# Performance work log

Measured on AMD Instinct MI355X. Metric: run time of the kernel, lower is better.

The kernel has to match this reference:

```python
import jax, jax.numpy as jnp
import numpy as np

N0, N1, N2 = 200000, 50000, 10000
D_IN, D_PROMPT, D_HID, D_OUT = 128, 64, 256, 2
E0, E1 = 800000, 160000


def _glorot(key, shape):
    fan_in, fan_out = shape[0], shape[1]
    lim = np.sqrt(6.0 / (fan_in + fan_out))
    return jax.random.uniform(key, shape, jnp.float32, -lim, lim)


def setup_inputs() -> dict:
    key = jax.random.key(0)
    ks = jax.random.split(key, 20)
    inp = {
        "features": jax.random.normal(ks[0], (N0, D_IN), jnp.float32),
        "membership_mask": jax.random.randint(ks[1], (N0,), 0, 2) > 0,
        "src0": jax.random.randint(ks[2], (E0,), 0, N0),
        "dst0": jax.random.randint(ks[3], (E0,), 0, N1),
        "src1": jax.random.randint(ks[4], (E1,), 0, N1),
        "dst1": jax.random.randint(ks[5], (E1,), 0, N2),
        "output_nodes_indices": jax.random.randint(ks[6], (N2,), 0, N2),
        # prompt MLPs
        "w_pin": _glorot(ks[7], (D_IN, D_PROMPT)),
        "b_pin": jnp.zeros((D_PROMPT,), jnp.float32),
        "w_pout": _glorot(ks[8], (D_IN, D_PROMPT)),
        "b_pout": jnp.zeros((D_PROMPT,), jnp.float32),
        # SAGEConv layer 0: (D_IN+D_PROMPT) -> D_HID
        "w_self0": _glorot(ks[9], (D_IN + D_PROMPT, D_HID)),
        "w_neigh0": _glorot(ks[10], (D_IN + D_PROMPT, D_HID)),
        "b0": jnp.zeros((D_HID,), jnp.float32),
        # SAGEConv layer 1: D_HID -> D_HID
        "w_self1": _glorot(ks[11], (D_HID, D_HID)),
        "w_neigh1": _glorot(ks[12], (D_HID, D_HID)),
        "b1": jnp.zeros((D_HID,), jnp.float32),
        # classifier
        "w_cls": _glorot(ks[13], (D_HID, D_OUT)),
        "b_cls": jnp.zeros((D_OUT,), jnp.float32),
    }
    return inp


def _sage_mean(h, src, dst, n_dst, w_self, w_neigh, b):
    # mean-aggregate src features into dst buckets (zero-degree -> 0, DGL semantics)
    agg = jax.ops.segment_sum(h[src], dst, num_segments=n_dst)
    deg = jax.ops.segment_sum(jnp.ones((src.shape[0],), h.dtype), dst, num_segments=n_dst)
    agg = agg / jnp.maximum(deg, 1.0)[:, None]
    return h[:n_dst] @ w_self + agg @ w_neigh + b


def reference(features, membership_mask, src0, dst0, src1, dst1, output_nodes_indices,
              w_pin, b_pin, w_pout, b_pout,
              w_self0, w_neigh0, b0, w_self1, w_neigh1, b1, w_cls, b_cls):
    p_in = jax.nn.relu(features @ w_pin + b_pin)
    p_out = jax.nn.relu(features @ w_pout + b_pout)
    sel = jnp.where(membership_mask[:, None], p_in, p_out)
    h = jnp.concatenate([features, sel], axis=1)          # [N0, D_IN+D_PROMPT]
    h = jax.nn.relu(_sage_mean(h, src0, dst0, N1, w_self0, w_neigh0, b0))  # [N1, D_HID]
    h = _sage_mean(h, src1, dst1, N2, w_self1, w_neigh1, b1)               # [N2, D_HID]
    logits = h @ w_cls + b_cls                             # [N2, D_OUT]
    return logits
```

## Files before the change

kernel.cpp:

```cpp
#include <hip/hip_runtime.h>


#define N0v 200000
#define N1v 50000
#define N2v 10000
#define E0v 800000
#define E1v 160000
#define TB0 49
#define TB1 10
#define TBL (TB0 + TB1)
#define NTILE 3125
#define PGRID 512

using u16 = unsigned short;
typedef __attribute__((ext_vector_type(8))) short short8;
typedef __attribute__((ext_vector_type(4))) float f32x4;

__device__ __forceinline__ float b2f(u16 u) {
    union { unsigned int i; float f; } v; v.i = ((unsigned int)u) << 16; return v.f;
}
__device__ __forceinline__ u16 f2b(float f) {
    union { float f; unsigned int i; } v; v.f = f;
    return (u16)((v.i + 0x7fffu + ((v.i >> 16) & 1u)) >> 16);
}
__device__ __forceinline__ void split2(float f, u16& h, u16& l) {
    h = f2b(f);
    l = f2b(f - b2f(h));
}

__global__ void k_prep(const unsigned* mask, int* flag,
                       const float* w_pin, const float* w_pout, u16* WTph, u16* WTpl,
                       const float* ws0, const float* wn0, u16* WT0h, u16* WT0l,
                       const float* ws1, const float* wn1, u16* WT1h, u16* WT1l,
                       const float* bc, float* outp,
                       const int* __restrict__ dst0, const int* __restrict__ dst1,
                       int* cnt0, int* cnt1, int* rk0, int* rk1) {
    const int R0 = 50000;
    const int R1 = R0 + 128 * 128;
    const int R2 = R1 + 256 * 384;
    const int R3 = R2 + 256 * 512;
    const int R4 = R3 + 2 * N2v;
    const int R5 = R4 + E0v;
    const int R6 = R5 + E1v;
    for (int i = blockIdx.x * blockDim.x + threadIdx.x; i < R6;
         i += gridDim.x * blockDim.x) {
        if (i < R0) {
            if (mask[i] > 1u) atomicOr(flag, 1);
        } else if (i < R1) {
            int j = i - R0, n = j >> 7, k = j & 127;
            float f = (n < 64) ? w_pin[k * 64 + n] : w_pout[k * 64 + (n - 64)];
            split2(f, WTph[j], WTpl[j]);
        } else if (i < R2) {
            int j = i - R1, n = j / 384, k = j % 384;
            float f = (k < 192) ? ws0[k * 256 + n] : wn0[(k - 192) * 256 + n];
            split2(f, WT0h[j], WT0l[j]);
        } else if (i < R3) {
            int j = i - R2, n = j >> 9, k = j & 511;
            float f = (k < 256) ? ws1[k * 256 + n] : wn1[(k - 256) * 256 + n];
            split2(f, WT1h[j], WT1l[j]);
        } else if (i < R4) {
            int j = i - R3;
            outp[j] = bc[j & 1];
        } else if (i < R5) {
            int e = i - R4;
            rk0[e] = atomicAdd(&cnt0[dst0[e]], 1);
        } else {
            int e = i - R5;
            rk1[e] = atomicAdd(&cnt1[dst1[e]], 1);
        }
    }
}

__global__ __launch_bounds__(256) void k_scan_a(const int* __restrict__ cnt0,
                                                int* __restrict__ off0,
                                                const int* __restrict__ cnt1,
                                                int* __restrict__ off1,
                                                int* __restrict__ tsum) {
    __shared__ int sd[256];
    const int t = threadIdx.x;
    const int blk = blockIdx.x;
    const int g1 = (blk >= TB0);
    const int b = g1 ? blk - TB0 : blk;
    const int n = g1 ? N2v : N1v;
    const int* cnt = g1 ? cnt1 : cnt0;
    int* off = g1 ? off1 : off0;
    const int i0 = b * 1024 + t * 4;
    int c[4] = {0, 0, 0, 0};
    if (i0 + 3 < n) {
        *(int4*)c = *(const int4*)&cnt[i0];
    } else {
        for (int j = 0; j < 4; j++) if (i0 + j < n) c[j] = cnt[i0 + j];
    }
    int s = c[0] + c[1] + c[2] + c[3];
    sd[t] = s;
    __syncthreads();
#pragma unroll
    for (int d = 1; d < 256; d <<= 1) {
        int v = (t >= d) ? sd[t - d] : 0;
        __syncthreads();
        sd[t] += v;
        __syncthreads();
    }
    int run = sd[t] - s;
    int o4[4];
#pragma unroll
    for (int j = 0; j < 4; j++) { o4[j] = run; run += c[j]; }
    if (i0 + 3 < n) *(int4*)&off[i0] = *(const int4*)o4;
    else for (int j = 0; j < 4; j++) if (i0 + j < n) off[i0 + j] = o4[j];
    if (t == 255) tsum[blk] = sd[255];
}

__global__ __launch_bounds__(256) void k_scan_c(int* __restrict__ off0,
                                                int* __restrict__ off1,
                                                const int* __restrict__ tsum) {
    __shared__ int lbase;
    const int t = threadIdx.x;
    const int blk = blockIdx.x;
    const int g1 = (blk >= TB0);
    const int b = g1 ? blk - TB0 : blk;
    const int n = g1 ? N2v : N1v;
    int* off = g1 ? off1 : off0;
    if (t < 64) {
        int v = (t < TBL) ? tsum[t] : 0;
        int incl = v;
#pragma unroll
        for (int d = 1; d < 64; d <<= 1) {
            int u = __shfl_up(incl, d);
            if (t >= d) incl += u;
        }
        int total0 = __shfl(incl, TB0 - 1);
        if (t == blk) lbase = (incl - v) - (g1 ? total0 : 0);
    }
    __syncthreads();
    const int base = lbase;
    const int i0 = b * 1024 + t * 4;
    if (i0 + 3 < n) {
        int4 v = *(int4*)&off[i0];
        v.x += base; v.y += base; v.z += base; v.w += base;
        *(int4*)&off[i0] = v;
    } else {
        for (int j = 0; j < 4; j++) if (i0 + j < n) off[i0 + j] += base;
    }
    if (blk == 0 && t == 0) { off0[N1v] = E0v; off1[N2v] = E1v; }
}

__global__ __launch_bounds__(256) void k_scatter2(
    const int* __restrict__ src0, const int* __restrict__ dst0,
    const int* __restrict__ off0, const int* __restrict__ rk0, int* __restrict__ ei0,
    const int* __restrict__ src1, const int* __restrict__ dst1,
    const int* __restrict__ off1, const int* __restrict__ rk1, int* __restrict__ ei1) {
    const int part = blockIdx.x & 7;
    const int chunk = blockIdx.x >> 3;
    const int nch = gridDim.x >> 3;
    {
        const int per = (E0v + nch - 1) / nch;
        const int i1 = min((chunk + 1) * per, E0v);
        for (int i = chunk * per + (int)threadIdx.x; i < i1; i += 256) {
            int d = dst0[i];
            if (d / 6250 == part) ei0[off0[d] + rk0[i]] = src0[i];
        }
    }
    {
        const int per = (E1v + nch - 1) / nch;
        const int i1 = min((chunk + 1) * per, E1v);
        for (int i = chunk * per + (int)threadIdx.x; i < i1; i += 256) {
            int d = dst1[i];
            if (d / 1250 == part) ei1[off1[d] + rk1[i]] = src1[i];
        }
    }
}

__global__ __launch_bounds__(256, 2) void k_gemm_p(
    const float* __restrict__ A, const u16* __restrict__ Bh, const u16* __restrict__ Bl,
    const float* __restrict__ b_pin, const float* __restrict__ b_pout,
    const void* maskp, const int* __restrict__ flag, u16* __restrict__ G) {
    __shared__ __align__(16) u16 STG[2][8448];
    __shared__ __align__(16) u16 EPI[8704];
    const int t = threadIdx.x;
    const int lane = t & 63, w = t >> 6;
    const int m = lane & 15, q = lane >> 4;
    const int colbase = w * 32;
    const int r15 = t >> 4, ch = t & 15;
    const int k0s = ch >> 2, q2s = ch & 3;

    const size_t ba = (size_t)(colbase + m) * 128 + q * 8;
    const size_t bb = (size_t)(colbase + 16 + m) * 128 + q * 8;
    short8 BfA[4][2], BfB[4][2];
#pragma unroll
    for (int k0 = 0; k0 < 4; k0++) {
        BfA[k0][0] = *(const short8*)&Bh[ba + k0 * 32];
        BfA[k0][1] = *(const short8*)&Bl[ba + k0 * 32];
        BfB[k0][0] = *(const short8*)&Bh[bb + k0 * 32];
        BfB[k0][1] = *(const short8*)&Bl[bb + k0 * 32];
    }
    const int fl = *flag;
    float bv0, bv1;
    {
        int c0 = colbase + m, c1 = colbase + 16 + m;
        bv0 = (c0 < 64) ? b_pin[c0] : b_pout[c0 - 64];
        bv1 = (c1 < 64) ? b_pin[c1] : b_pout[c1 - 64];
    }

    float4 va[8];
    {
        const float* ap = &A[(size_t)(blockIdx.x * 64 + r15) * 128 + ch * 8];
#pragma unroll
        for (int p = 0; p < 4; p++) {
            va[2 * p]     = *(const float4*)(ap + (size_t)p * 16 * 128);
            va[2 * p + 1] = *(const float4*)(ap + (size_t)p * 16 * 128 + 4);
        }
    }

    int buf = 0;
    for (int bm = blockIdx.x; bm < NTILE; bm += PGRID, buf ^= 1) {
        const int r0 = bm * 64;
        u16* stg = STG[buf];
#pragma unroll
        for (int p = 0; p < 4; p++) {
            u16 h8[8];
            h8[0] = f2b(va[2 * p].x); h8[1] = f2b(va[2 * p].y);
            h8[2] = f2b(va[2 * p].z); h8[3] = f2b(va[2 * p].w);
            h8[4] = f2b(va[2 * p + 1].x); h8[5] = f2b(va[2 * p + 1].y);
            h8[6] = f2b(va[2 * p + 1].z); h8[7] = f2b(va[2 * p + 1].w);
            *(uint4*)&stg[((p * 4 + k0s) * 66 + 16 * q2s + r15) * 8] = *(const uint4*)h8;
        }
        __syncthreads();

        if (bm + PGRID < NTILE) {
            const float* ap = &A[(size_t)((bm + PGRID) * 64 + r15) * 128 + ch * 8];
#pragma unroll
            for (int p = 0; p < 4; p++) {
                va[2 * p]     = *(const float4*)(ap + (size_t)p * 16 * 128);
                va[2 * p + 1] = *(const float4*)(ap + (size_t)p * 16 * 128 + 4);
            }
        }
        bool mk0, mk1;
        {
            const int ra = r0 + (t >> 3), rb = ra + 32;
            if (fl) {
                mk0 = ((const unsigned char*)maskp)[ra] != 0;
                mk1 = ((const unsigned char*)maskp)[rb] != 0;
            } else {
                mk0 = ((const int*)maskp)[ra] != 0;
                mk1 = ((const int*)maskp)[rb] != 0;
            }
        }

        f32x4 acc[4][2] = {};
#pragma unroll
        for (int k0 = 0; k0 < 4; k0++) {
#pragma unroll
            for (int mi = 0; mi < 4; mi++) {
                short8 af = *(const short8*)&stg[((mi * 4 + k0) * 66 + lane) * 8];
                acc[mi][0] = __builtin_amdgcn_mfma_f32_16x16x32_bf16(af, BfA[k0][0], acc[mi][0], 0, 0, 0);
                acc[mi][0] = __builtin_amdgcn_mfma_f32_16x16x32_bf16(af, BfA[k0][1], acc[mi][0], 0, 0, 0);
                acc[mi][1] = __builtin_amdgcn_mfma_f32_16x16x32_bf16(af, BfB[k0][0], acc[mi][1], 0, 0, 0);
                acc[mi][1] = __builtin_amdgcn_mfma_f32_16x16x32_bf16(af, BfB[k0][1], acc[mi][1], 0, 0, 0);
            }
        }

#pragma unroll
        for (int mi = 0; mi < 4; mi++)
#pragma unroll
            for (int r = 0; r < 4; r++) {
                float v0 = acc[mi][0][r] + bv0;
                float v1 = acc[mi][1][r] + bv1;
                v0 = v0 > 0.f ? v0 : 0.f;
                v1 = v1 > 0.f ? v1 : 0.f;
                EPI[(mi * 16 + q * 4 + r) * 136 + colbase + m] = f2b(v0);
                EPI[(mi * 16 + q * 4 + r) * 136 + colbase + 16 + m] = f2b(v1);
            }
        __syncthreads();

        {
            const int c8 = t & 7;
            const int rt = t >> 3;
            *(uint4*)&G[(size_t)(r0 + rt) * 192 + 128 + c8 * 8] =
                *(const uint4*)&EPI[rt * 136 + (mk0 ? 0 : 64) + c8 * 8];
            *(uint4*)&G[(size_t)(r0 + 32 + rt) * 192 + 128 + c8 * 8] =
                *(const uint4*)&EPI[(32 + rt) * 136 + (mk1 ? 0 : 64) + c8 * 8];
        }
#pragma unroll
        for (int p = 0; p < 4; p++) {
            uint4 v = *(const uint4*)&stg[((p * 4 + k0s) * 66 + 16 * q2s + r15) * 8];
            *(uint4*)&G[(size_t)(r0 + r15 + 16 * p) * 192 + ch * 8] = v;
        }
    }
}

template <int MODE, int KT, int SEGA0, int MT>
__global__ __launch_bounds__(256, 3) void k_g(
    const u16* __restrict__ A0, int s0, const u16* __restrict__ A1, int s1,
    const u16* __restrict__ Bh, const u16* __restrict__ Bl,
    const float* __restrict__ bias,
    u16* __restrict__ CH, float* __restrict__ outp, const float* __restrict__ wc,
    int M) {
    constexpr int MI = MT / 16;
    __shared__ __align__(16) u16 LA[MI * KT * 66 * 8];
    const int t = threadIdx.x;
    const int bm = blockIdx.x >> 1, bn = blockIdx.x & 1;
    const int lane = t & 63, w = t >> 6;
    const int m = lane & 15, q = lane >> 4;
    const int r0 = bm * MT;
    const int colbase = bn * 128 + w * 32;
    const int K = KT * 32;

    {
        constexpr int TPR = 256 / MT;
        constexpr int SPT = KT / TPR;
        const int rr = t / TPR, sub = t & (TPR - 1);
        int arow = r0 + rr; if (arow >= M) arow = M - 1;
        const int mi = rr >> 4, r15 = rr & 15;
#pragma unroll
        for (int s = 0; s < SPT; s++) {
            const int kc = sub * SPT + s;
#pragma unroll
            for (int q2 = 0; q2 < 4; q2++) {
                const int c = kc * 32 + q2 * 8;
                uint4 v = (c < SEGA0)
                              ? *(const uint4*)&A0[(size_t)arow * s0 + c]
                              : *(const uint4*)&A1[(size_t)arow * s1 + (c - SEGA0)];
                *(uint4*)&LA[((mi * KT + kc) * 66 + 16 * q2 + r15) * 8] = v;
            }
        }
    }
    __syncthreads();

    const size_t ba = (size_t)(colbase + m) * K + q * 8;
    const size_t bb = (size_t)(colbase + 16 + m) * K + q * 8;

    f32x4 acc[MI][2] = {};
#pragma unroll 1
    for (int kb = 0; kb < KT; kb += 4) {
#pragma unroll
        for (int k0 = 0; k0 < 4; k0++) {
            const size_t ko = (size_t)(kb + k0) * 32;
            short8 b0h = *(const short8*)&Bh[ba + ko];
            short8 b0l = *(const short8*)&Bl[ba + ko];
            short8 b1h = *(const short8*)&Bh[bb + ko];
            short8 b1l = *(const short8*)&Bl[bb + ko];
#pragma unroll
            for (int mi = 0; mi < MI; mi++) {
                short8 af = *(const short8*)&LA[((mi * KT + kb + k0) * 66 + lane) * 8];
                acc[mi][0] = __builtin_amdgcn_mfma_f32_16x16x32_bf16(af, b0h, acc[mi][0], 0, 0, 0);
                acc[mi][0] = __builtin_amdgcn_mfma_f32_16x16x32_bf16(af, b0l, acc[mi][0], 0, 0, 0);
                acc[mi][1] = __builtin_amdgcn_mfma_f32_16x16x32_bf16(af, b1h, acc[mi][1], 0, 0, 0);
                acc[mi][1] = __builtin_amdgcn_mfma_f32_16x16x32_bf16(af, b1l, acc[mi][1], 0, 0, 0);
            }
        }
    }

    if (MODE == 1) {
        float bv[2];
#pragma unroll
        for (int nt = 0; nt < 2; nt++) bv[nt] = bias[colbase + nt * 16 + m];
        __syncthreads();
#pragma unroll
        for (int mi = 0; mi < MI; mi++)
#pragma unroll
            for (int nt = 0; nt < 2; nt++)
#pragma unroll
                for (int r = 0; r < 4; r++) {
                    float v = acc[mi][nt][r] + bv[nt];
                    v = v > 0.f ? v : 0.f;
                    LA[(mi * 16 + q * 4 + r) * 136 + w * 32 + nt * 16 + m] = f2b(v);
                }
        __syncthreads();
        const int c16 = t & 15;
#pragma unroll
        for (int pass = 0; pass < MT / 16; pass++) {
            const int rt = pass * 16 + (t >> 4);
            const int row = r0 + rt;
            if (row < M) {
                *(uint4*)&CH[(size_t)row * 256 + bn * 128 + c16 * 8] =
                    *(const uint4*)&LA[rt * 136 + c16 * 8];
            }
        }
    } else {
        const int ca = colbase + m, cb = colbase + 16 + m;
        const float bva = bias[ca], bvb = bias[cb];
        const float w0a = wc[ca * 2], w1a = wc[ca * 2 + 1];
        const float w0b = wc[cb * 2], w1b = wc[cb * 2 + 1];
#pragma unroll
        for (int mi = 0; mi < MI; mi++) {
#pragma unroll
            for (int r = 0; r < 4; r++) {
                int row = r0 + mi * 16 + q * 4 + r;
                float va = acc[mi][0][r] + bva;
                float vb = acc[mi][1][r] + bvb;
                float p0 = va * w0a + vb * w0b;
                float p1 = va * w1a + vb * w1b;
#pragma unroll
                for (int s = 1; s < 16; s <<= 1) {
                    p0 += __shfl_xor(p0, s);
                    p1 += __shfl_xor(p1, s);
                }
                if (m == 0 && row < M) {
                    atomicAdd(&outp[row * 2], p0);
                    atomicAdd(&outp[row * 2 + 1], p1);
                }
            }
        }
    }
}

__global__ void k_agg0(const u16* __restrict__ G, const int* __restrict__ off,
                       const int* __restrict__ eidx, u16* __restrict__ aggH) {
    int wid = (blockIdx.x * blockDim.x + threadIdx.x) >> 6;
    int lane = threadIdx.x & 63;
    if (wid >= N1v) return;
    int b = off[wid], e = off[wid + 1];
    float f0 = 0.f, f1 = 0.f, p0 = 0.f;
    for (int base = b; base < e; base += 64) {
        int li = base + lane;
        int idx = eidx[li < e ? li : (e - 1)];
        int nch = e - base; if (nch > 64) nch = 64;
        int j = 0;
        for (; j + 4 <= nch; j += 4) {
            int sa = __shfl(idx, j), sb = __shfl(idx, j + 1);
            int sc = __shfl(idx, j + 2), sd = __shfl(idx, j + 3);
            const u16* ra = &G[(size_t)sa * 192];
            const u16* rb = &G[(size_t)sb * 192];
            const u16* rc = &G[(size_t)sc * 192];
            const u16* rd = &G[(size_t)sd * 192];
            unsigned fa = *(const unsigned*)&ra[2 * lane];
            unsigned fb = *(const unsigned*)&rb[2 * lane];
            unsigned fc = *(const unsigned*)&rc[2 * lane];
            unsigned fd = *(const unsigned*)&rd[2 * lane];
            u16 pa = ra[128 + lane], pb = rb[128 + lane];
            u16 pc = rc[128 + lane], pd = rd[128 + lane];
            f0 += b2f((u16)fa) + b2f((u16)fb) + b2f((u16)fc) + b2f((u16)fd);
            f1 += b2f((u16)(fa >> 16)) + b2f((u16)(fb >> 16)) +
                  b2f((u16)(fc >> 16)) + b2f((u16)(fd >> 16));
            p0 += b2f(pa) + b2f(pb) + b2f(pc) + b2f(pd);
        }
        for (; j < nch; j++) {
            int s = __shfl(idx, j);
            const u16* row = &G[(size_t)s * 192];
            unsigned fv = *(const unsigned*)&row[2 * lane];
            f0 += b2f((u16)fv);
            f1 += b2f((u16)(fv >> 16));
            p0 += b2f(row[128 + lane]);
        }
    }
    int deg = e - b;
    float inv = 1.0f / (float)(deg > 1 ? deg : 1);
    size_t rb2 = (size_t)wid * 192;
    *(unsigned*)&aggH[rb2 + 2 * lane] =
        (unsigned)f2b(f0 * inv) | ((unsigned)f2b(f1 * inv) << 16);
    aggH[rb2 + 128 + lane] = f2b(p0 * inv);
}

__global__ void k_agg1(const u16* __restrict__ h1H, const int* __restrict__ off,
                       const int* __restrict__ eidx, u16* __restrict__ aggH) {
    int wid = (blockIdx.x * blockDim.x + threadIdx.x) >> 6;
    int lane = threadIdx.x & 63;
    if (wid >= N2v) return;
    int b = off[wid], e = off[wid + 1];
    float a0 = 0.f, a1 = 0.f, a2 = 0.f, a3 = 0.f;
    for (int base = b; base < e; base += 64) {
        int li = base + lane;
        int idx = eidx[li < e ? li : (e - 1)];
        int nch = e - base; if (nch > 64) nch = 64;
        int j = 0;
        for (; j + 4 <= nch; j += 4) {
            int sa = __shfl(idx, j), sb = __shfl(idx, j + 1);
            int sc = __shfl(idx, j + 2), sd = __shfl(idx, j + 3);
            const u16* ra = &h1H[(size_t)sa * 256];
            const u16* rb = &h1H[(size_t)sb * 256];
            const u16* rc = &h1H[(size_t)sc * 256];
            const u16* rd = &h1H[(size_t)sd * 256];
            unsigned va0 = *(const unsigned*)&ra[2 * lane];
            unsigned vb0 = *(const unsigned*)&rb[2 * lane];
            unsigned vc0 = *(const unsigned*)&rc[2 * lane];
            unsigned vd0 = *(const unsigned*)&rd[2 * lane];
            unsigned va1 = *(const unsigned*)&ra[128 + 2 * lane];
            unsigned vb1 = *(const unsigned*)&rb[128 + 2 * lane];
            unsigned vc1 = *(const unsigned*)&rc[128 + 2 * lane];
            unsigned vd1 = *(const unsigned*)&rd[128 + 2 * lane];
            a0 += b2f((u16)va0) + b2f((u16)vb0) + b2f((u16)vc0) + b2f((u16)vd0);
            a1 += b2f((u16)(va0 >> 16)) + b2f((u16)(vb0 >> 16)) +
                  b2f((u16)(vc0 >> 16)) + b2f((u16)(vd0 >> 16));
            a2 += b2f((u16)va1) + b2f((u16)vb1) + b2f((u16)vc1) + b2f((u16)vd1);
            a3 += b2f((u16)(va1 >> 16)) + b2f((u16)(vb1 >> 16)) +
                  b2f((u16)(vc1 >> 16)) + b2f((u16)(vd1 >> 16));
        }
        for (; j < nch; j++) {
            int s = __shfl(idx, j);
            const u16* row = &h1H[(size_t)s * 256];
            unsigned v0 = *(const unsigned*)&row[2 * lane];
            unsigned v1 = *(const unsigned*)&row[128 + 2 * lane];
            a0 += b2f((u16)v0); a1 += b2f((u16)(v0 >> 16));
            a2 += b2f((u16)v1); a3 += b2f((u16)(v1 >> 16));
        }
    }
    int deg = e - b;
    float inv = 1.0f / (float)(deg > 1 ? deg : 1);
    size_t rb2 = (size_t)wid * 256;
    *(unsigned*)&aggH[rb2 + 2 * lane] =
        (unsigned)f2b(a0 * inv) | ((unsigned)f2b(a1 * inv) << 16);
    *(unsigned*)&aggH[rb2 + 128 + 2 * lane] =
        (unsigned)f2b(a2 * inv) | ((unsigned)f2b(a3 * inv) << 16);
}

extern "C" void kernel_launch(void* const* d_in, const int* in_sizes, int n_in,
                              void* d_out, int out_size, void* d_ws, size_t ws_size,
                              hipStream_t stream) {
    const float* features = (const float*)d_in[0];
    const void* maskp     = d_in[1];
    const int* src0       = (const int*)d_in[2];
    const int* dst0       = (const int*)d_in[3];
    const int* src1       = (const int*)d_in[4];
    const int* dst1       = (const int*)d_in[5];
    const float* w_pin    = (const float*)d_in[7];
    const float* b_pin    = (const float*)d_in[8];
    const float* w_pout   = (const float*)d_in[9];
    const float* b_pout   = (const float*)d_in[10];
    const float* w_self0  = (const float*)d_in[11];
    const float* w_neigh0 = (const float*)d_in[12];
    const float* b0       = (const float*)d_in[13];
    const float* w_self1  = (const float*)d_in[14];
    const float* w_neigh1 = (const float*)d_in[15];
    const float* b1       = (const float*)d_in[16];
    const float* w_cls    = (const float*)d_in[17];
    const float* b_cls    = (const float*)d_in[18];
    float* out = (float*)d_out;
    (void)in_sizes; (void)n_in; (void)out_size; (void)ws_size;

    char* ws = (char*)d_ws;
    size_t o = 0;
    auto alloc = [&](size_t bytes) { size_t r = o; o += (bytes + 255) & ~(size_t)255; return r; };
    size_t o_flag = alloc(4);
    size_t o_cnt0 = alloc(N1v * 4);
    size_t o_cnt1 = alloc(N2v * 4);
    size_t zero_end = o;
    size_t o_G    = alloc((size_t)N0v * 192 * 2);
    size_t o_aggH = alloc((size_t)N1v * 192 * 2);
    size_t o_h1H  = alloc((size_t)N1v * 256 * 2);
    size_t o_ag1H = alloc((size_t)N2v * 256 * 2);
    size_t o_wtph = alloc(128 * 128 * 2), o_wtpl = alloc(128 * 128 * 2);
    size_t o_wt0h = alloc(256 * 384 * 2), o_wt0l = alloc(256 * 384 * 2);
    size_t o_wt1h = alloc(256 * 512 * 2), o_wt1l = alloc(256 * 512 * 2);
    size_t o_off0 = alloc((N1v + 1) * 4);
    size_t o_off1 = alloc((N2v + 1) * 4);
    size_t o_ei0  = alloc((size_t)E0v * 4);
    size_t o_ei1  = alloc((size_t)E1v * 4);
    size_t o_rk0  = alloc((size_t)E0v * 4);
    size_t o_rk1  = alloc((size_t)E1v * 4);
    size_t o_tsum = alloc(TBL * 4);

    int* flag = (int*)(ws + o_flag);
    int* cnt0 = (int*)(ws + o_cnt0);
    int* cnt1 = (int*)(ws + o_cnt1);
    u16* G     = (u16*)(ws + o_G);
    u16* aggH  = (u16*)(ws + o_aggH);
    u16* h1H   = (u16*)(ws + o_h1H);
    u16* ag1H  = (u16*)(ws + o_ag1H);
    u16* WTph = (u16*)(ws + o_wtph);
    u16* WTpl = (u16*)(ws + o_wtpl);
    u16* WT0h = (u16*)(ws + o_wt0h);
    u16* WT0l = (u16*)(ws + o_wt0l);
    u16* WT1h = (u16*)(ws + o_wt1h);
    u16* WT1l = (u16*)(ws + o_wt1l);
    int* off0 = (int*)(ws + o_off0);
    int* off1 = (int*)(ws + o_off1);
    int* ei0  = (int*)(ws + o_ei0);
    int* ei1  = (int*)(ws + o_ei1);
    int* rk0  = (int*)(ws + o_rk0);
    int* rk1  = (int*)(ws + o_rk1);
    int* tsum = (int*)(ws + o_tsum);

    hipMemsetAsync(ws + o_flag, 0, zero_end - o_flag, stream);

    k_prep<<<1024, 256, 0, stream>>>((const unsigned*)maskp, flag,
                                     w_pin, w_pout, WTph, WTpl,
                                     w_self0, w_neigh0, WT0h, WT0l,
                                     w_self1, w_neigh1, WT1h, WT1l,
                                     b_cls, out, dst0, dst1, cnt0, cnt1, rk0, rk1);

    k_scan_a<<<TBL, 256, 0, stream>>>(cnt0, off0, cnt1, off1, tsum);
    k_scan_c<<<TBL, 256, 0, stream>>>(off0, off1, tsum);

    k_scatter2<<<2048, 256, 0, stream>>>(src0, dst0, off0, rk0, ei0,
                                         src1, dst1, off1, rk1, ei1);

    k_gemm_p<<<PGRID, 256, 0, stream>>>(features, WTph, WTpl,
                                        b_pin, b_pout, maskp, flag, G);

    k_agg0<<<(N1v + 3) / 4, 256, 0, stream>>>(G, off0, ei0, aggH);

    k_g<1, 12, 192, 64><<<((N1v + 63) / 64) * 2, 256, 0, stream>>>(
        G, 192, aggH, 192, WT0h, WT0l, b0, h1H, nullptr, nullptr, N1v);

    k_agg1<<<(N2v + 3) / 4, 256, 0, stream>>>(h1H, off1, ei1, ag1H);

    k_g<3, 16, 256, 32><<<((N2v + 31) / 32) * 2, 256, 0, stream>>>(
        h1H, 256, ag1H, 256, WT1h, WT1l, b1, nullptr, out, w_cls, N2v);
}
```

Baseline: 413.2 us.

## Merge prompt GEMM with prep work into one heterogeneous kernel

Splits the old prep kernel so that mask-type detection runs in its own small kernel. Weight splitting, output init and edge counting move into extra blocks of the prompt GEMM kernel, so they run alongside the features GEMM instead of before it. The prompt weights are now split into hi/lo bf16 parts directly in registers inside the GEMM blocks, which removes the transposed prompt-weight buffers. The trade-off is one extra small launch plus strided global weight loads repeated by each GEMM block, and prep blocks compete with GEMM blocks for CUs.

```diff
diff --git a/kernel.cpp b/kernel.cpp
--- a/kernel.cpp
+++ b/kernel.cpp
@@ -11,6 +11,7 @@
 #define TBL (TB0 + TB1)
 #define NTILE 3125
 #define PGRID 512
+#define PREPB 768
 
 using u16 = unsigned short;
 typedef __attribute__((ext_vector_type(8))) short short8;
@@ -28,45 +29,178 @@
     l = f2b(f - b2f(h));
 }
 
-__global__ void k_prep(const unsigned* mask, int* flag,
-                       const float* w_pin, const float* w_pout, u16* WTph, u16* WTpl,
-                       const float* ws0, const float* wn0, u16* WT0h, u16* WT0l,
-                       const float* ws1, const float* wn1, u16* WT1h, u16* WT1l,
-                       const float* bc, float* outp,
-                       const int* __restrict__ dst0, const int* __restrict__ dst1,
-                       int* cnt0, int* cnt1, int* rk0, int* rk1) {
-    const int R0 = 50000;
-    const int R1 = R0 + 128 * 128;
-    const int R2 = R1 + 256 * 384;
-    const int R3 = R2 + 256 * 512;
-    const int R4 = R3 + 2 * N2v;
-    const int R5 = R4 + E0v;
-    const int R6 = R5 + E1v;
-    for (int i = blockIdx.x * blockDim.x + threadIdx.x; i < R6;
+__global__ void k_detect(const unsigned* mask, int* flag) {
+    for (int i = blockIdx.x * blockDim.x + threadIdx.x; i < 50000;
          i += gridDim.x * blockDim.x) {
-        if (i < R0) {
-            if (mask[i] > 1u) atomicOr(flag, 1);
-        } else if (i < R1) {
-            int j = i - R0, n = j >> 7, k = j & 127;
-            float f = (n < 64) ? w_pin[k * 64 + n] : w_pout[k * 64 + (n - 64)];
-            split2(f, WTph[j], WTpl[j]);
-        } else if (i < R2) {
-            int j = i - R1, n = j / 384, k = j % 384;
-            float f = (k < 192) ? ws0[k * 256 + n] : wn0[(k - 192) * 256 + n];
-            split2(f, WT0h[j], WT0l[j]);
-        } else if (i < R3) {
-            int j = i - R2, n = j >> 9, k = j & 511;
-            float f = (k < 256) ? ws1[k * 256 + n] : wn1[(k - 256) * 256 + n];
-            split2(f, WT1h[j], WT1l[j]);
-        } else if (i < R4) {
-            int j = i - R3;
-            outp[j] = bc[j & 1];
-        } else if (i < R5) {
-            int e = i - R4;
-            rk0[e] = atomicAdd(&cnt0[dst0[e]], 1);
-        } else {
-            int e = i - R5;
-            rk1[e] = atomicAdd(&cnt1[dst1[e]], 1);
+        if (mask[i] > 1u) atomicOr(flag, 1);
+    }
+}
+
+__global__ __launch_bounds__(256, 2) void k_mega(
+    const float* __restrict__ A, const float* __restrict__ w_pin,
+    const float* __restrict__ w_pout,
+    const float* __restrict__ b_pin, const float* __restrict__ b_pout,
+    const void* maskp, const int* __restrict__ flag, u16* __restrict__ G,
+    const float* __restrict__ ws0, const float* __restrict__ wn0,
+    u16* WT0h, u16* WT0l,
+    const float* __restrict__ ws1, const float* __restrict__ wn1,
+    u16* WT1h, u16* WT1l,
+    const float* __restrict__ bc, float* outp,
+    const int* __restrict__ dst0, const int* __restrict__ dst1,
+    int* cnt0, int* cnt1, int* rk0, int* rk1) {
+    __shared__ __align__(16) u16 STG[2][8448];
+    __shared__ __align__(16) u16 EPI[8704];
+    const int t = threadIdx.x;
+
+    if (blockIdx.x >= PGRID) {
+        const int R1 = 256 * 384;
+        const int R2 = R1 + 256 * 512;
+        const int R3 = R2 + 2 * N2v;
+        const int R4 = R3 + E0v;
+        const int R5 = R4 + E1v;
+        const int stride = PREPB * 256;
+        for (int i = (blockIdx.x - PGRID) * 256 + t; i < R5; i += stride) {
+            if (i < R1) {
+                int n = i / 384, k = i % 384;
+                float f = (k < 192) ? ws0[k * 256 + n] : wn0[(k - 192) * 256 + n];
+                split2(f, WT0h[i], WT0l[i]);
+            } else if (i < R2) {
+                int j = i - R1, n = j >> 9, k = j & 511;
+                float f = (k < 256) ? ws1[k * 256 + n] : wn1[(k - 256) * 256 + n];
+                split2(f, WT1h[j], WT1l[j]);
+            } else if (i < R3) {
+                int j = i - R2;
+                outp[j] = bc[j & 1];
+            } else if (i < R4) {
+                int e = i - R3;
+                rk0[e] = atomicAdd(&cnt0[dst0[e]], 1);
+            } else {
+                int e = i - R4;
+                rk1[e] = atomicAdd(&cnt1[dst1[e]], 1);
+            }
+        }
+        return;
+    }
+
+    const int lane = t & 63, w = t >> 6;
+    const int m = lane & 15, q = lane >> 4;
+    const int colbase = w * 32;
+    const int r15 = t >> 4, ch = t & 15;
+    const int k0s = ch >> 2, q2s = ch & 3;
+
+    short8 BfA[4][2], BfB[4][2];
+    {
+        const int c0 = colbase + m, c1 = colbase + 16 + m;
+        const float* wp0 = (c0 < 64) ? w_pin : w_pout;
+        const int cc0 = (c0 < 64) ? c0 : c0 - 64;
+        const float* wp1 = (c1 < 64) ? w_pin : w_pout;
+        const int cc1 = (c1 < 64) ? c1 : c1 - 64;
+#pragma unroll
+        for (int k0 = 0; k0 < 4; k0++) {
+            u16 h8[8], l8[8];
+#pragma unroll
+            for (int j = 0; j < 8; j++)
+                split2(wp0[(k0 * 32 + q * 8 + j) * 64 + cc0], h8[j], l8[j]);
+            BfA[k0][0] = *(const short8*)h8;
+            BfA[k0][1] = *(const short8*)l8;
+#pragma unroll
+            for (int j = 0; j < 8; j++)
+                split2(wp1[(k0 * 32 + q * 8 + j) * 64 + cc1], h8[j], l8[j]);
+            BfB[k0][0] = *(const short8*)h8;
+            BfB[k0][1] = *(const short8*)l8;
+        }
+    }
+    const int fl = *flag;
+    float bv0, bv1;
+    {
+        int c0 = colbase + m, c1 = colbase + 16 + m;
+        bv0 = (c0 < 64) ? b_pin[c0] : b_pout[c0 - 64];
+        bv1 = (c1 < 64) ? b_pin[c1] : b_pout[c1 - 64];
+    }
+
+    float4 va[8];
+    {
+        const float* ap = &A[(size_t)(blockIdx.x * 64 + r15) * 128 + ch * 8];
+#pragma unroll
+        for (int p = 0; p < 4; p++) {
+            va[2 * p]     = *(const float4*)(ap + (size_t)p * 16 * 128);
+            va[2 * p + 1] = *(const float4*)(ap + (size_t)p * 16 * 128 + 4);
+        }
+    }
+
+    int buf = 0;
+    for (int bm = blockIdx.x; bm < NTILE; bm += PGRID, buf ^= 1) {
+        const int r0 = bm * 64;
+        u16* stg = STG[buf];
+#pragma unroll
+        for (int p = 0; p < 4; p++) {
+            u16 h8[8];
+            h8[0] = f2b(va[2 * p].x); h8[1] = f2b(va[2 * p].y);
+            h8[2] = f2b(va[2 * p].z); h8[3] = f2b(va[2 * p].w);
+            h8[4] = f2b(va[2 * p + 1].x); h8[5] = f2b(va[2 * p + 1].y);
+            h8[6] = f2b(va[2 * p + 1].z); h8[7] = f2b(va[2 * p + 1].w);
+            *(uint4*)&stg[((p * 4 + k0s) * 66 + 16 * q2s + r15) * 8] = *(const uint4*)h8;
+        }
+        __syncthreads();
+
+        if (bm + PGRID < NTILE) {
+            const float* ap = &A[(size_t)((bm + PGRID) * 64 + r15) * 128 + ch * 8];
+#pragma unroll
+            for (int p = 0; p < 4; p++) {
+                va[2 * p]     = *(const float4*)(ap + (size_t)p * 16 * 128);
+                va[2 * p + 1] = *(const float4*)(ap + (size_t)p * 16 * 128 + 4);
+            }
+        }
+        bool mk0, mk1;
+        {
+            const int ra = r0 + (t >> 3), rb = ra + 32;
+            if (fl) {
+                mk0 = ((const unsigned char*)maskp)[ra] != 0;
+                mk1 = ((const unsigned char*)maskp)[rb] != 0;
+            } else {
+                mk0 = ((const int*)maskp)[ra] != 0;
+                mk1 = ((const int*)maskp)[rb] != 0;
+            }
+        }
+
+        f32x4 acc[4][2] = {};
+#pragma unroll
+        for (int k0 = 0; k0 < 4; k0++) {
+#pragma unroll
+            for (int mi = 0; mi < 4; mi++) {
+                short8 af = *(const short8*)&stg[((mi * 4 + k0) * 66 + lane) * 8];
+                acc[mi][0] = __builtin_amdgcn_mfma_f32_16x16x32_bf16(af, BfA[k0][0], acc[mi][0], 0, 0, 0);
+                acc[mi][0] = __builtin_amdgcn_mfma_f32_16x16x32_bf16(af, BfA[k0][1], acc[mi][0], 0, 0, 0);
+                acc[mi][1] = __builtin_amdgcn_mfma_f32_16x16x32_bf16(af, BfB[k0][0], acc[mi][1], 0, 0, 0);
+                acc[mi][1] = __builtin_amdgcn_mfma_f32_16x16x32_bf16(af, BfB[k0][1], acc[mi][1], 0, 0, 0);
+            }
+        }
+
+#pragma unroll
+        for (int mi = 0; mi < 4; mi++)
+#pragma unroll
+            for (int r = 0; r < 4; r++) {
+                float v0 = acc[mi][0][r] + bv0;
+                float v1 = acc[mi][1][r] + bv1;
+                v0 = v0 > 0.f ? v0 : 0.f;
+                v1 = v1 > 0.f ? v1 : 0.f;
+                EPI[(mi * 16 + q * 4 + r) * 136 + colbase + m] = f2b(v0);
+                EPI[(mi * 16 + q * 4 + r) * 136 + colbase + 16 + m] = f2b(v1);
+            }
+        __syncthreads();
+
+        {
+            const int c8 = t & 7;
+            const int rt = t >> 3;
+            *(uint4*)&G[(size_t)(r0 + rt) * 192 + 128 + c8 * 8] =
+                *(const uint4*)&EPI[rt * 136 + (mk0 ? 0 : 64) + c8 * 8];
+            *(uint4*)&G[(size_t)(r0 + 32 + rt) * 192 + 128 + c8 * 8] =
+                *(const uint4*)&EPI[(32 + rt) * 136 + (mk1 ? 0 : 64) + c8 * 8];
+        }
+#pragma unroll
+        for (int p = 0; p < 4; p++) {
+            uint4 v = *(const uint4*)&stg[((p * 4 + k0s) * 66 + 16 * q2s + r15) * 8];
+            *(uint4*)&G[(size_t)(r0 + r15 + 16 * p) * 192 + ch * 8] = v;
         }
     }
 }
@@ -166,124 +300,6 @@
         for (int i = chunk * per + (int)threadIdx.x; i < i1; i += 256) {
             int d = dst1[i];
             if (d / 1250 == part) ei1[off1[d] + rk1[i]] = src1[i];
-        }
-    }
-}
-
-__global__ __launch_bounds__(256, 2) void k_gemm_p(
-    const float* __restrict__ A, const u16* __restrict__ Bh, const u16* __restrict__ Bl,
-    const float* __restrict__ b_pin, const float* __restrict__ b_pout,
-    const void* maskp, const int* __restrict__ flag, u16* __restrict__ G) {
-    __shared__ __align__(16) u16 STG[2][8448];
-    __shared__ __align__(16) u16 EPI[8704];
-    const int t = threadIdx.x;
-    const int lane = t & 63, w = t >> 6;
-    const int m = lane & 15, q = lane >> 4;
-    const int colbase = w * 32;
-    const int r15 = t >> 4, ch = t & 15;
-    const int k0s = ch >> 2, q2s = ch & 3;
-
-    const size_t ba = (size_t)(colbase + m) * 128 + q * 8;
-    const size_t bb = (size_t)(colbase + 16 + m) * 128 + q * 8;
-    short8 BfA[4][2], BfB[4][2];
-#pragma unroll
-    for (int k0 = 0; k0 < 4; k0++) {
-        BfA[k0][0] = *(const short8*)&Bh[ba + k0 * 32];
-        BfA[k0][1] = *(const short8*)&Bl[ba + k0 * 32];
-        BfB[k0][0] = *(const short8*)&Bh[bb + k0 * 32];
-        BfB[k0][1] = *(const short8*)&Bl[bb + k0 * 32];
-    }
-    const int fl = *flag;
-    float bv0, bv1;
-    {
-        int c0 = colbase + m, c1 = colbase + 16 + m;
-        bv0 = (c0 < 64) ? b_pin[c0] : b_pout[c0 - 64];
-        bv1 = (c1 < 64) ? b_pin[c1] : b_pout[c1 - 64];
-    }
-
-    float4 va[8];
-    {
-        const float* ap = &A[(size_t)(blockIdx.x * 64 + r15) * 128 + ch * 8];
-#pragma unroll
-        for (int p = 0; p < 4; p++) {
-            va[2 * p]     = *(const float4*)(ap + (size_t)p * 16 * 128);
-            va[2 * p + 1] = *(const float4*)(ap + (size_t)p * 16 * 128 + 4);
-        }
-    }
-
-    int buf = 0;
-    for (int bm = blockIdx.x; bm < NTILE; bm += PGRID, buf ^= 1) {
-        const int r0 = bm * 64;
-        u16* stg = STG[buf];
-#pragma unroll
-        for (int p = 0; p < 4; p++) {
-            u16 h8[8];
-            h8[0] = f2b(va[2 * p].x); h8[1] = f2b(va[2 * p].y);
-            h8[2] = f2b(va[2 * p].z); h8[3] = f2b(va[2 * p].w);
-            h8[4] = f2b(va[2 * p + 1].x); h8[5] = f2b(va[2 * p + 1].y);
-            h8[6] = f2b(va[2 * p + 1].z); h8[7] = f2b(va[2 * p + 1].w);
-            *(uint4*)&stg[((p * 4 + k0s) * 66 + 16 * q2s + r15) * 8] = *(const uint4*)h8;
-        }
-        __syncthreads();
-
-        if (bm + PGRID < NTILE) {
-            const float* ap = &A[(size_t)((bm + PGRID) * 64 + r15) * 128 + ch * 8];
-#pragma unroll
-            for (int p = 0; p < 4; p++) {
-                va[2 * p]     = *(const float4*)(ap + (size_t)p * 16 * 128);
-                va[2 * p + 1] = *(const float4*)(ap + (size_t)p * 16 * 128 + 4);
-            }
-        }
-        bool mk0, mk1;
-        {
-            const int ra = r0 + (t >> 3), rb = ra + 32;
-            if (fl) {
-                mk0 = ((const unsigned char*)maskp)[ra] != 0;
-                mk1 = ((const unsigned char*)maskp)[rb] != 0;
-            } else {
-                mk0 = ((const int*)maskp)[ra] != 0;
-                mk1 = ((const int*)maskp)[rb] != 0;
-            }
-        }
-
-        f32x4 acc[4][2] = {};
-#pragma unroll
-        for (int k0 = 0; k0 < 4; k0++) {
-#pragma unroll
-            for (int mi = 0; mi < 4; mi++) {
-                short8 af = *(const short8*)&stg[((mi * 4 + k0) * 66 + lane) * 8];
-                acc[mi][0] = __builtin_amdgcn_mfma_f32_16x16x32_bf16(af, BfA[k0][0], acc[mi][0], 0, 0, 0);
-                acc[mi][0] = __builtin_amdgcn_mfma_f32_16x16x32_bf16(af, BfA[k0][1], acc[mi][0], 0, 0, 0);
-                acc[mi][1] = __builtin_amdgcn_mfma_f32_16x16x32_bf16(af, BfB[k0][0], acc[mi][1], 0, 0, 0);
-                acc[mi][1] = __builtin_amdgcn_mfma_f32_16x16x32_bf16(af, BfB[k0][1], acc[mi][1], 0, 0, 0);
-            }
-        }
-
-#pragma unroll
-        for (int mi = 0; mi < 4; mi++)
-#pragma unroll
-            for (int r = 0; r < 4; r++) {
-                float v0 = acc[mi][0][r] + bv0;
-                float v1 = acc[mi][1][r] + bv1;
-                v0 = v0 > 0.f ? v0 : 0.f;
-                v1 = v1 > 0.f ? v1 : 0.f;
-                EPI[(mi * 16 + q * 4 + r) * 136 + colbase + m] = f2b(v0);
-                EPI[(mi * 16 + q * 4 + r) * 136 + colbase + 16 + m] = f2b(v1);
-            }
-        __syncthreads();
-
-        {
-            const int c8 = t & 7;
-            const int rt = t >> 3;
-            *(uint4*)&G[(size_t)(r0 + rt) * 192 + 128 + c8 * 8] =
-                *(const uint4*)&EPI[rt * 136 + (mk0 ? 0 : 64) + c8 * 8];
-            *(uint4*)&G[(size_t)(r0 + 32 + rt) * 192 + 128 + c8 * 8] =
-                *(const uint4*)&EPI[(32 + rt) * 136 + (mk1 ? 0 : 64) + c8 * 8];
-        }
-#pragma unroll
-        for (int p = 0; p < 4; p++) {
-            uint4 v = *(const uint4*)&stg[((p * 4 + k0s) * 66 + 16 * q2s + r15) * 8];
-            *(uint4*)&G[(size_t)(r0 + r15 + 16 * p) * 192 + ch * 8] = v;
         }
     }
 }
@@ -538,7 +554,6 @@
     size_t o_aggH = alloc((size_t)N1v * 192 * 2);
     size_t o_h1H  = alloc((size_t)N1v * 256 * 2);
     size_t o_ag1H = alloc((size_t)N2v * 256 * 2);
-    size_t o_wtph = alloc(128 * 128 * 2), o_wtpl = alloc(128 * 128 * 2);
     size_t o_wt0h = alloc(256 * 384 * 2), o_wt0l = alloc(256 * 384 * 2);
     size_t o_wt1h = alloc(256 * 512 * 2), o_wt1l = alloc(256 * 512 * 2);
     size_t o_off0 = alloc((N1v + 1) * 4);
@@ -556,8 +571,6 @@
     u16* aggH  = (u16*)(ws + o_aggH);
     u16* h1H   = (u16*)(ws + o_h1H);
     u16* ag1H  = (u16*)(ws + o_ag1H);
-    u16* WTph = (u16*)(ws + o_wtph);
-    u16* WTpl = (u16*)(ws + o_wtpl);
     u16* WT0h = (u16*)(ws + o_wt0h);
     u16* WT0l = (u16*)(ws + o_wt0l);
     u16* WT1h = (u16*)(ws + o_wt1h);
@@ -572,11 +585,12 @@
 
     hipMemsetAsync(ws + o_flag, 0, zero_end - o_flag, stream);
 
-    k_prep<<<1024, 256, 0, stream>>>((const unsigned*)maskp, flag,
-                                     w_pin, w_pout, WTph, WTpl,
-                                     w_self0, w_neigh0, WT0h, WT0l,
-                                     w_self1, w_neigh1, WT1h, WT1l,
-                                     b_cls, out, dst0, dst1, cnt0, cnt1, rk0, rk1);
+    k_detect<<<64, 256, 0, stream>>>((const unsigned*)maskp, flag);
+
+    k_mega<<<PGRID + PREPB, 256, 0, stream>>>(
+        features, w_pin, w_pout, b_pin, b_pout, maskp, flag, G,
+        w_self0, w_neigh0, WT0h, WT0l, w_self1, w_neigh1, WT1h, WT1l,
+        b_cls, out, dst0, dst1, cnt0, cnt1, rk0, rk1);
 
     k_scan_a<<<TBL, 256, 0, stream>>>(cnt0, off0, cnt1, off1, tsum);
     k_scan_c<<<TBL, 256, 0, stream>>>(off0, off1, tsum);
@@ -584,9 +598,6 @@
     k_scatter2<<<2048, 256, 0, stream>>>(src0, dst0, off0, rk0, ei0,
                                          src1, dst1, off1, rk1, ei1);
 
-    k_gemm_p<<<PGRID, 256, 0, stream>>>(features, WTph, WTpl,
-                                        b_pin, b_pout, maskp, flag, G);
-
     k_agg0<<<(N1v + 3) / 4, 256, 0, stream>>>(G, off0, ei0, aggH);
 
     k_g<1, 12, 192, 64><<<((N1v + 63) / 64) * 2, 256, 0, stream>>>(
```

New measurement: 418.6 us. Within noise of the previous version (+1.3%).

## Split prep kernel into weight-prep blocks and XCD-partitioned degree counting

Applied to the files above, without the earlier changes.

Dedicates 64 blocks to the weight transposition, bf16 split, mask check and output-bias init. The remaining 2048 blocks count degrees, grouped into 8 parts that each handle only destinations in one range. Each part reads all edges in its chunk but only does atomics for its own destination range, so a given counter's atomics come from blocks that likely share an XCD/L2 on the 8-XCD chip. This is meant to cut cross-die atomic contention, at the cost of reading the dst arrays eight times.

```diff
diff --git a/kernel.cpp b/kernel.cpp
--- a/kernel.cpp
+++ b/kernel.cpp
@@ -28,45 +28,61 @@
     l = f2b(f - b2f(h));
 }
 
-__global__ void k_prep(const unsigned* mask, int* flag,
-                       const float* w_pin, const float* w_pout, u16* WTph, u16* WTpl,
-                       const float* ws0, const float* wn0, u16* WT0h, u16* WT0l,
-                       const float* ws1, const float* wn1, u16* WT1h, u16* WT1l,
-                       const float* bc, float* outp,
-                       const int* __restrict__ dst0, const int* __restrict__ dst1,
-                       int* cnt0, int* cnt1, int* rk0, int* rk1) {
-    const int R0 = 50000;
-    const int R1 = R0 + 128 * 128;
-    const int R2 = R1 + 256 * 384;
-    const int R3 = R2 + 256 * 512;
-    const int R4 = R3 + 2 * N2v;
-    const int R5 = R4 + E0v;
-    const int R6 = R5 + E1v;
-    for (int i = blockIdx.x * blockDim.x + threadIdx.x; i < R6;
-         i += gridDim.x * blockDim.x) {
-        if (i < R0) {
-            if (mask[i] > 1u) atomicOr(flag, 1);
-        } else if (i < R1) {
-            int j = i - R0, n = j >> 7, k = j & 127;
-            float f = (n < 64) ? w_pin[k * 64 + n] : w_pout[k * 64 + (n - 64)];
-            split2(f, WTph[j], WTpl[j]);
-        } else if (i < R2) {
-            int j = i - R1, n = j / 384, k = j % 384;
-            float f = (k < 192) ? ws0[k * 256 + n] : wn0[(k - 192) * 256 + n];
-            split2(f, WT0h[j], WT0l[j]);
-        } else if (i < R3) {
-            int j = i - R2, n = j >> 9, k = j & 511;
-            float f = (k < 256) ? ws1[k * 256 + n] : wn1[(k - 256) * 256 + n];
-            split2(f, WT1h[j], WT1l[j]);
-        } else if (i < R4) {
-            int j = i - R3;
-            outp[j] = bc[j & 1];
-        } else if (i < R5) {
-            int e = i - R4;
-            rk0[e] = atomicAdd(&cnt0[dst0[e]], 1);
-        } else {
-            int e = i - R5;
-            rk1[e] = atomicAdd(&cnt1[dst1[e]], 1);
+__global__ __launch_bounds__(256) void k_prep(
+    const unsigned* mask, int* flag,
+    const float* w_pin, const float* w_pout, u16* WTph, u16* WTpl,
+    const float* ws0, const float* wn0, u16* WT0h, u16* WT0l,
+    const float* ws1, const float* wn1, u16* WT1h, u16* WT1l,
+    const float* bc, float* outp,
+    const int* __restrict__ dst0, const int* __restrict__ dst1,
+    int* cnt0, int* cnt1, int* rk0, int* rk1) {
+    const int bid = blockIdx.x;
+    const int t = threadIdx.x;
+    if (bid < 64) {
+        const int R0 = 50000;
+        const int R1 = R0 + 128 * 128;
+        const int R2 = R1 + 256 * 384;
+        const int R3 = R2 + 256 * 512;
+        const int R4 = R3 + 2 * N2v;
+        for (int i = bid * 256 + t; i < R4; i += 64 * 256) {
+            if (i < R0) {
+                if (mask[i] > 1u) atomicOr(flag, 1);
+            } else if (i < R1) {
+                int j = i - R0, n = j >> 7, k = j & 127;
+                float f = (n < 64) ? w_pin[k * 64 + n] : w_pout[k * 64 + (n - 64)];
+                split2(f, WTph[j], WTpl[j]);
+            } else if (i < R2) {
+                int j = i - R1, n = j / 384, k = j % 384;
+                float f = (k < 192) ? ws0[k * 256 + n] : wn0[(k - 192) * 256 + n];
+                split2(f, WT0h[j], WT0l[j]);
+            } else if (i < R3) {
+                int j = i - R2, n = j >> 9, k = j & 511;
+                float f = (k < 256) ? ws1[k * 256 + n] : wn1[(k - 256) * 256 + n];
+                split2(f, WT1h[j], WT1l[j]);
+            } else {
+                int j = i - R3;
+                outp[j] = bc[j & 1];
+            }
+        }
+        return;
+    }
+    const int part = (bid - 64) & 7;
+    const int chunk = (bid - 64) >> 3;
+    const int nch = (gridDim.x - 64) >> 3;
+    {
+        const int per = (E0v + nch - 1) / nch;
+        const int i1 = min((chunk + 1) * per, E0v);
+        for (int i = chunk * per + t; i < i1; i += 256) {
+            int d = dst0[i];
+            if (d / 6250 == part) rk0[i] = atomicAdd(&cnt0[d], 1);
+        }
+    }
+    {
+        const int per = (E1v + nch - 1) / nch;
+        const int i1 = min((chunk + 1) * per, E1v);
+        for (int i = chunk * per + t; i < i1; i += 256) {
+            int d = dst1[i];
+            if (d / 1250 == part) rk1[i] = atomicAdd(&cnt1[d], 1);
         }
     }
 }
@@ -572,7 +588,7 @@
 
     hipMemsetAsync(ws + o_flag, 0, zero_end - o_flag, stream);
 
-    k_prep<<<1024, 256, 0, stream>>>((const unsigned*)maskp, flag,
+    k_prep<<<2112, 256, 0, stream>>>((const unsigned*)maskp, flag,
                                      w_pin, w_pout, WTph, WTpl,
                                      w_self0, w_neigh0, WT0h, WT0l,
                                      w_self1, w_neigh1, WT1h, WT1l,
```

Result: no change. 420.4 us (+1.8%).
